# Optimization experiments

Hardware: AMD Instinct MI355X
Metric: run time of the kernel (lower is better)

## Reference

```python
import jax, jax.numpy as jnp
import numpy as np

N, E, G = 50000, 1600000, 8
IN, H, C = 64, 4, 32
HID = H * C  # 128
L = 3


def setup_inputs() -> dict:
    key = jax.random.key(0)
    ks = jax.random.split(key, 20)
    x = jax.random.normal(ks[0], (N, IN), dtype=jnp.float32)
    edge_index = jax.random.randint(ks[1], (2, E), 0, N, dtype=jnp.int64)
    batch = jnp.sort(jax.random.randint(ks[2], (N,), 0, G, dtype=jnp.int64))
    s = 0.05
    Wp = jax.random.normal(ks[3], (IN, HID), dtype=jnp.float32) * s
    bp = jnp.zeros((HID,), dtype=jnp.float32)
    Wl = jax.random.normal(ks[4], (L, HID, HID), dtype=jnp.float32) * s
    att_src = jax.random.normal(ks[5], (L, H, C), dtype=jnp.float32) * s
    att_dst = jax.random.normal(ks[6], (L, H, C), dtype=jnp.float32) * s
    bconv = jnp.zeros((L, HID), dtype=jnp.float32)
    W1 = jax.random.normal(ks[7], (2 * HID, 256), dtype=jnp.float32) * s
    b1 = jnp.zeros((256,), dtype=jnp.float32)
    W2 = jax.random.normal(ks[8], (256, 128), dtype=jnp.float32) * s
    b2 = jnp.zeros((128,), dtype=jnp.float32)
    W3 = jax.random.normal(ks[9], (128, 1), dtype=jnp.float32) * s
    b3 = jnp.zeros((1,), dtype=jnp.float32)
    return dict(x=x, edge_index=edge_index, batch=batch, Wp=Wp, bp=bp, Wl=Wl,
                att_src=att_src, att_dst=att_dst, bconv=bconv,
                W1=W1, b1=b1, W2=W2, b2=b2, W3=W3, b3=b3)


def _gat_layer(x, src, dst, W, a_src, a_dst, b):
    # PyG GATConv (concat=True, add_self_loops handled by caller via src/dst)
    h = (x @ W).reshape(N, H, C)                      # [N,H,C]
    asrc = jnp.sum(h * a_src, axis=-1)                # [N,H]
    adst = jnp.sum(h * a_dst, axis=-1)                # [N,H]
    e = jax.nn.leaky_relu(asrc[src] + adst[dst], 0.2)  # [E',H]
    m = jax.ops.segment_max(e, dst, num_segments=N)   # scatter-softmax over dst
    e = jnp.exp(e - m[dst])
    z = jax.ops.segment_sum(e, dst, num_segments=N)
    alpha = e / (z[dst] + 1e-16)                      # [E',H]
    out = jax.ops.segment_sum(h[src] * alpha[:, :, None], dst, num_segments=N)
    return out.reshape(N, HID) + b


def reference(x, edge_index, batch, Wp, bp, Wl, att_src, att_dst, bconv,
              W1, b1, W2, b2, W3, b3):
    # add self loops once (PyG default add_self_loops=True)
    loop = jnp.arange(N, dtype=edge_index.dtype)
    src = jnp.concatenate([edge_index[0], loop])
    dst = jnp.concatenate([edge_index[1], loop])

    h = jax.nn.relu(x @ Wp + bp)
    for l in range(L):
        h = jax.nn.relu(_gat_layer(h, src, dst, Wl[l], att_src[l], att_dst[l], bconv[l]))

    cnt = jax.ops.segment_sum(jnp.ones((N,), h.dtype), batch, num_segments=G)
    mean = jax.ops.segment_sum(h, batch, num_segments=G) / jnp.maximum(cnt, 1.0)[:, None]
    mx = jax.ops.segment_max(h, batch, num_segments=G)
    mx = jnp.where(cnt[:, None] > 0, mx, 0.0)
    p = jnp.concatenate([mean, mx], axis=-1)          # [G, 2*HID]

    p = jax.nn.relu(p @ W1 + b1)
    p = jax.nn.relu(p @ W2 + b2)
    return (p @ W3 + b3).squeeze(-1)                  # [G]
```

## Files before the change

kernel.cpp:

```cpp
#include <hip/hip_runtime.h>
#include <math.h>

#define NN 50000
#define GG 8
#define HEADS 4
#define CH 32
#define HID 128
#define NLAYER 3
#define POOL_S 64
#define DEG_CAP 96
#define NBG2 ((NN + 63) / 64)
#define NBS 1024

typedef __attribute__((ext_vector_type(8))) short bf16x8;
typedef __attribute__((ext_vector_type(4))) float f32x4;

__device__ float g_h[(size_t)NN * HID];
__device__ __attribute__((aligned(16))) unsigned short g_h2b[(size_t)NN * HID];
__device__ __attribute__((aligned(16))) unsigned short g_xhi[(size_t)NN * HID];
__device__ __attribute__((aligned(16))) unsigned short g_xlo[(size_t)NN * HID];
__device__ __attribute__((aligned(16))) unsigned short g_wthi[(size_t)NLAYER * HID * HID];
__device__ __attribute__((aligned(16))) unsigned short g_wtlo[(size_t)NLAYER * HID * HID];
__device__ float g_as[(size_t)NN * HEADS];
__device__ float g_ad[(size_t)NN * HEADS];
__device__ int g_cursor[NN];
__device__ __attribute__((aligned(16))) unsigned short g_csr16[(size_t)NN * DEG_CAP];
__device__ int g_starts[GG + 1];
__device__ double g_psum[(size_t)GG * POOL_S * HID];
__device__ float g_pmax[(size_t)GG * POOL_S * HID];

__device__ __forceinline__ float lrelu(float v) { return v > 0.f ? v : 0.2f * v; }

__device__ __forceinline__ float bf2f(unsigned short u) {
    union { unsigned int i; float f; } v;
    v.i = ((unsigned int)u) << 16;
    return v.f;
}
__device__ __forceinline__ unsigned short f2bf(float f) {
    union { float f; unsigned int i; } v;
    v.f = f;
    unsigned int r = v.i + 0x7FFFu + ((v.i >> 16) & 1u);
    return (unsigned short)(r >> 16);
}

__global__ void zero_kernel() {
    int i = blockIdx.x * blockDim.x + threadIdx.x;
    if (i < NN) g_cursor[i] = 0;
}

__global__ void wprep_kernel(const float* __restrict__ Wl) {
    int idx = blockIdx.x * 256 + threadIdx.x;
    if (idx >= NLAYER * HID * HID) return;
    int lay = idx / (HID * HID);
    int rem = idx - lay * HID * HID;
    int n = rem >> 7, k = rem & 127;
    float v = Wl[(size_t)lay * HID * HID + (size_t)k * HID + n];
    unsigned short h = f2bf(v);
    float r = v - bf2f(h);
    g_wthi[idx] = h;
    g_wtlo[idx] = f2bf(r);
}

template <int K>
__device__ __forceinline__ void proj_body(
    const float* __restrict__ Xp, const float* __restrict__ W, const float* __restrict__ bias,
    int blk) {
    constexpr int KT = 32;
    constexpr int XS = 68;
    __shared__ float Ws[KT * 128];
    __shared__ float Xs[KT * XS];
    int tid = threadIdx.x;
    int base = blk * 64;
    int rows = NN - base;
    if (rows > 64) rows = 64;
    int cg = tid & 15, rg = tid >> 4;
    int c0 = cg * 8, r0 = rg * 4;
    float acc[4][8];
#pragma unroll
    for (int i = 0; i < 4; i++)
#pragma unroll
        for (int j = 0; j < 8; j++) acc[i][j] = 0.f;

    for (int kb = 0; kb < K; kb += KT) {
        {
            const float4* Wg = (const float4*)(W + (size_t)kb * 128);
            float4* Ws4 = (float4*)Ws;
#pragma unroll
            for (int u = 0; u < 4; u++) Ws4[tid + u * 256] = Wg[tid + u * 256];
        }
#pragma unroll
        for (int u = 0; u < 2; u++) {
            int i = tid + u * 256;
            int r = i >> 3, k4 = i & 7;
            float4 v = {0.f, 0.f, 0.f, 0.f};
            if (r < rows) v = *(const float4*)(Xp + (size_t)(base + r) * K + kb + k4 * 4);
            Xs[(k4 * 4 + 0) * XS + r] = v.x;
            Xs[(k4 * 4 + 1) * XS + r] = v.y;
            Xs[(k4 * 4 + 2) * XS + r] = v.z;
            Xs[(k4 * 4 + 3) * XS + r] = v.w;
        }
        __syncthreads();
#pragma unroll 8
        for (int k = 0; k < KT; k++) {
            const float4 xa = *(const float4*)&Xs[k * XS + r0];
            const float4 wa = *(const float4*)&Ws[k * 128 + c0];
            const float4 wb = *(const float4*)&Ws[k * 128 + c0 + 4];
            const float xr[4] = {xa.x, xa.y, xa.z, xa.w};
            const float wr[8] = {wa.x, wa.y, wa.z, wa.w, wb.x, wb.y, wb.z, wb.w};
#pragma unroll
            for (int ii = 0; ii < 4; ii++)
#pragma unroll
                for (int jj = 0; jj < 8; jj++) acc[ii][jj] += xr[ii] * wr[jj];
        }
        __syncthreads();
    }

    float bv[8];
#pragma unroll
    for (int j = 0; j < 8; j++) bv[j] = bias[c0 + j];
#pragma unroll
    for (int ii = 0; ii < 4; ii++) {
        int r = r0 + ii;
        if (r < rows) {
            ushort4 h0, l0, h1, l1;
            float o[8];
#pragma unroll
            for (int jj = 0; jj < 8; jj++) o[jj] = fmaxf(acc[ii][jj] + bv[jj], 0.f);
            h0.x = f2bf(o[0]); h0.y = f2bf(o[1]); h0.z = f2bf(o[2]); h0.w = f2bf(o[3]);
            h1.x = f2bf(o[4]); h1.y = f2bf(o[5]); h1.z = f2bf(o[6]); h1.w = f2bf(o[7]);
            l0.x = f2bf(o[0] - bf2f(h0.x)); l0.y = f2bf(o[1] - bf2f(h0.y));
            l0.z = f2bf(o[2] - bf2f(h0.z)); l0.w = f2bf(o[3] - bf2f(h0.w));
            l1.x = f2bf(o[4] - bf2f(h1.x)); l1.y = f2bf(o[5] - bf2f(h1.y));
            l1.z = f2bf(o[6] - bf2f(h1.z)); l1.w = f2bf(o[7] - bf2f(h1.w));
            size_t off = (size_t)(base + r) * 128 + c0;
            *(ushort4*)&g_xhi[off] = h0;
            *(ushort4*)&g_xhi[off + 4] = h1;
            *(ushort4*)&g_xlo[off] = l0;
            *(ushort4*)&g_xlo[off + 4] = l1;
        }
    }
}

__device__ __forceinline__ void mfma_att_body(
    const float* __restrict__ att_s, const float* __restrict__ att_d,
    int lay, int blk) {
    __shared__ float Ysh[64][HID];
    int tid = threadIdx.x;
    int w = tid >> 6, l = tid & 63;
    int base = blk * 64;
    int rows = NN - base;
    if (rows > 64) rows = 64;
    int ar = l & 15, kg = l >> 4;
    int arow = base + w * 16 + ar;
    if (arow >= NN) arow = NN - 1;
    const unsigned short* xh = g_xhi + (size_t)arow * HID + kg * 8;
    const unsigned short* xl = g_xlo + (size_t)arow * HID + kg * 8;
    const unsigned short* wh = g_wthi + (size_t)lay * HID * HID + (size_t)ar * HID + kg * 8;
    const unsigned short* wl = g_wtlo + (size_t)lay * HID * HID + (size_t)ar * HID + kg * 8;

    f32x4 acc[8];
#pragma unroll
    for (int ct = 0; ct < 8; ct++) acc[ct] = (f32x4){0.f, 0.f, 0.f, 0.f};

#pragma unroll
    for (int ks = 0; ks < 4; ks++) {
        bf16x8 ah = *(const bf16x8*)(xh + ks * 32);
        bf16x8 al = *(const bf16x8*)(xl + ks * 32);
#pragma unroll
        for (int ct = 0; ct < 8; ct++) {
            bf16x8 bh = *(const bf16x8*)(wh + ct * 16 * HID + ks * 32);
            bf16x8 bl = *(const bf16x8*)(wl + ct * 16 * HID + ks * 32);
            acc[ct] = __builtin_amdgcn_mfma_f32_16x16x32_bf16(ah, bh, acc[ct], 0, 0, 0);
            acc[ct] = __builtin_amdgcn_mfma_f32_16x16x32_bf16(al, bh, acc[ct], 0, 0, 0);
            acc[ct] = __builtin_amdgcn_mfma_f32_16x16x32_bf16(ah, bl, acc[ct], 0, 0, 0);
        }
    }

#pragma unroll
    for (int ct = 0; ct < 8; ct++)
#pragma unroll
        for (int j = 0; j < 4; j++)
            Ysh[w * 16 + kg * 4 + j][ct * 16 + ar] = acc[ct][j];
    __syncthreads();

    int cg = tid & 15, rg = tid >> 4;
    int c0 = cg * 8, r0 = rg * 4;
    float avs[8], avd[8];
#pragma unroll
    for (int j = 0; j < 8; j++) { avs[j] = att_s[c0 + j]; avd[j] = att_d[c0 + j]; }
#pragma unroll
    for (int ii = 0; ii < 4; ii++) {
        int r = r0 + ii;
        float o[8];
#pragma unroll
        for (int jj = 0; jj < 8; jj++) o[jj] = Ysh[r][c0 + jj];
        if (r < rows) {
            uint4 pk;
            pk.x = (unsigned)f2bf(o[0]) | ((unsigned)f2bf(o[1]) << 16);
            pk.y = (unsigned)f2bf(o[2]) | ((unsigned)f2bf(o[3]) << 16);
            pk.z = (unsigned)f2bf(o[4]) | ((unsigned)f2bf(o[5]) << 16);
            pk.w = (unsigned)f2bf(o[6]) | ((unsigned)f2bf(o[7]) << 16);
            *(uint4*)&g_h2b[(size_t)(base + r) * 128 + c0] = pk;
        }
        float ps = 0.f, pd = 0.f;
#pragma unroll
        for (int jj = 0; jj < 8; jj++) { ps += o[jj] * avs[jj]; pd += o[jj] * avd[jj]; }
        ps += __shfl_xor(ps, 1); ps += __shfl_xor(ps, 2);
        pd += __shfl_xor(pd, 1); pd += __shfl_xor(pd, 2);
        if ((cg & 3) == 0 && r < rows) {
            g_as[(size_t)(base + r) * 4 + (cg >> 2)] = ps;
            g_ad[(size_t)(base + r) * 4 + (cg >> 2)] = pd;
        }
    }
}

__device__ __forceinline__ void scatter_body(
    const int* __restrict__ srcv, const int* __restrict__ dstv,
    int ebeg, int eend, int blk, int nblk) {
    int idx = ebeg + blk * 256 + threadIdx.x;
    int stride = nblk * 256;
    for (int j = idx; j < eend; j += stride) {
        int d = dstv[j];
        int pos = atomicAdd(&g_cursor[d], 1);
        if (pos < DEG_CAP) g_csr16[(size_t)d * DEG_CAP + pos] = (unsigned short)srcv[j];
    }
}

__global__ __launch_bounds__(256) void fat1_kernel(
    const float* __restrict__ Xp, const float* __restrict__ W, const float* __restrict__ bias,
    const int* __restrict__ srcv, const int* __restrict__ dstv, int ebeg, int eend) {
    if (blockIdx.x < NBG2) proj_body<64>(Xp, W, bias, blockIdx.x);
    else scatter_body(srcv, dstv, ebeg, eend, blockIdx.x - NBG2, gridDim.x - NBG2);
}

__global__ __launch_bounds__(256, 2) void fat2_kernel(
    const float* __restrict__ att_s, const float* __restrict__ att_d,
    const int* __restrict__ srcv, const int* __restrict__ dstv, int ebeg, int eend) {
    if (blockIdx.x < NBG2) mfma_att_body(att_s, att_d, 0, blockIdx.x);
    else scatter_body(srcv, dstv, ebeg, eend, blockIdx.x - NBG2, gridDim.x - NBG2);
}

__global__ __launch_bounds__(256, 2) void att_gemm_kernel(
    const float* __restrict__ att_s, const float* __restrict__ att_d, int lay) {
    mfma_att_body(att_s, att_d, lay, blockIdx.x);
}

template <bool LAST>
__global__ __launch_bounds__(256) void gat_layer_kernel(const float* __restrict__ bconv) {
    int wave = threadIdx.x >> 6;
    int lane = threadIdx.x & 63;
    int i = blockIdx.x * 4 + wave;

    int deg = g_cursor[i];
    if (deg > DEG_CAP) deg = DEG_CAP;

    int stream = lane >> 5;
    int sl = lane & 31;
    int hl = sl >> 3;
    int li = sl & 7;
    int c0 = sl * 4;
    int bsel = lane & 56;

    float ad_h = g_ad[(size_t)i * 4 + hl];
    const unsigned short* csr = &g_csr16[(size_t)i * DEG_CAP];

    float4 acc = {0.f, 0.f, 0.f, 0.f};
    float zraw = 0.f;

    int nfull = deg >> 4;
    for (int t = 0; t < nfull; ++t) {
        int j0 = t * 16 + stream * 8;
        uint4 cs = *(const uint4*)(csr + j0);
        int s0 = cs.x & 0xFFFF, s1 = cs.x >> 16;
        int s2 = cs.y & 0xFFFF, s3 = cs.y >> 16;
        int s4 = cs.z & 0xFFFF, s5 = cs.z >> 16;
        int s6 = cs.w & 0xFFFF, s7 = cs.w >> 16;
        ushort4 q0 = *(const ushort4*)&g_h2b[(s0 << 7) + c0];
        ushort4 q1 = *(const ushort4*)&g_h2b[(s1 << 7) + c0];
        ushort4 q2 = *(const ushort4*)&g_h2b[(s2 << 7) + c0];
        ushort4 q3 = *(const ushort4*)&g_h2b[(s3 << 7) + c0];
        ushort4 q4 = *(const ushort4*)&g_h2b[(s4 << 7) + c0];
        ushort4 q5 = *(const ushort4*)&g_h2b[(s5 << 7) + c0];
        ushort4 q6 = *(const ushort4*)&g_h2b[(s6 << 7) + c0];
        ushort4 q7 = *(const ushort4*)&g_h2b[(s7 << 7) + c0];
        unsigned wsel = li < 4 ? (li < 2 ? cs.x : cs.y) : (li < 6 ? cs.z : cs.w);
        int sm = (li & 1) ? (int)(wsel >> 16) : (int)(wsel & 0xFFFF);
        float a = g_as[(sm << 2) + hl];
        float wr = expf(lrelu(a + ad_h));
        zraw += wr;
        float w0 = __shfl(wr, bsel | 0);
        float w1 = __shfl(wr, bsel | 1);
        float w2 = __shfl(wr, bsel | 2);
        float w3 = __shfl(wr, bsel | 3);
        float w4 = __shfl(wr, bsel | 4);
        float w5 = __shfl(wr, bsel | 5);
        float w6 = __shfl(wr, bsel | 6);
        float w7 = __shfl(wr, bsel | 7);
        acc.x += w0 * bf2f(q0.x); acc.y += w0 * bf2f(q0.y); acc.z += w0 * bf2f(q0.z); acc.w += w0 * bf2f(q0.w);
        acc.x += w1 * bf2f(q1.x); acc.y += w1 * bf2f(q1.y); acc.z += w1 * bf2f(q1.z); acc.w += w1 * bf2f(q1.w);
        acc.x += w2 * bf2f(q2.x); acc.y += w2 * bf2f(q2.y); acc.z += w2 * bf2f(q2.z); acc.w += w2 * bf2f(q2.w);
        acc.x += w3 * bf2f(q3.x); acc.y += w3 * bf2f(q3.y); acc.z += w3 * bf2f(q3.z); acc.w += w3 * bf2f(q3.w);
        acc.x += w4 * bf2f(q4.x); acc.y += w4 * bf2f(q4.y); acc.z += w4 * bf2f(q4.z); acc.w += w4 * bf2f(q4.w);
        acc.x += w5 * bf2f(q5.x); acc.y += w5 * bf2f(q5.y); acc.z += w5 * bf2f(q5.z); acc.w += w5 * bf2f(q5.w);
        acc.x += w6 * bf2f(q6.x); acc.y += w6 * bf2f(q6.y); acc.z += w6 * bf2f(q6.z); acc.w += w6 * bf2f(q6.w);
        acc.x += w7 * bf2f(q7.x); acc.y += w7 * bf2f(q7.y); acc.z += w7 * bf2f(q7.z); acc.w += w7 * bf2f(q7.w);
    }

    int tbase = nfull * 16 + stream * 8;
#pragma unroll
    for (int k = 0; k < 8; ++k) {
        if (tbase + k < deg) {
            int s = csr[tbase + k];
            float a = g_as[(s << 2) + hl];
            float wr = expf(lrelu(a + ad_h));
            zraw += wr * 0.125f;
            ushort4 q = *(const ushort4*)&g_h2b[(s << 7) + c0];
            acc.x += wr * bf2f(q.x); acc.y += wr * bf2f(q.y);
            acc.z += wr * bf2f(q.z); acc.w += wr * bf2f(q.w);
        }
    }

    acc.x += __shfl_xor(acc.x, 32);
    acc.y += __shfl_xor(acc.y, 32);
    acc.z += __shfl_xor(acc.z, 32);
    acc.w += __shfl_xor(acc.w, 32);
    zraw += __shfl_xor(zraw, 1);
    zraw += __shfl_xor(zraw, 2);
    zraw += __shfl_xor(zraw, 4);
    zraw += __shfl_xor(zraw, 32);

    if (lane < 32) {
        float as_i = g_as[(i << 2) + hl];
        float sw = expf(lrelu(as_i + ad_h));
        float invz = 1.f / (zraw + sw + 1e-16f);
        ushort4 qs = *(const ushort4*)&g_h2b[(i << 7) + c0];
        float4 bc = *(const float4*)&bconv[c0];
        float4 o;
        o.x = fmaxf((sw * bf2f(qs.x) + acc.x) * invz + bc.x, 0.f);
        o.y = fmaxf((sw * bf2f(qs.y) + acc.y) * invz + bc.y, 0.f);
        o.z = fmaxf((sw * bf2f(qs.z) + acc.z) * invz + bc.z, 0.f);
        o.w = fmaxf((sw * bf2f(qs.w) + acc.w) * invz + bc.w, 0.f);
        if (LAST) {
            *(float4*)&g_h[(size_t)i * 128 + c0] = o;
        } else {
            ushort4 hh, ll;
            hh.x = f2bf(o.x); hh.y = f2bf(o.y); hh.z = f2bf(o.z); hh.w = f2bf(o.w);
            ll.x = f2bf(o.x - bf2f(hh.x)); ll.y = f2bf(o.y - bf2f(hh.y));
            ll.z = f2bf(o.z - bf2f(hh.z)); ll.w = f2bf(o.w - bf2f(hh.w));
            *(ushort4*)&g_xhi[(size_t)i * 128 + c0] = hh;
            *(ushort4*)&g_xlo[(size_t)i * 128 + c0] = ll;
        }
    }
}

__global__ void bounds_kernel(const int* __restrict__ batch) {
    int t = threadIdx.x;
    if (t > GG) return;
    int lo = 0, hi = NN;
    while (lo < hi) {
        int mid = (lo + hi) >> 1;
        if (batch[mid] < t) lo = mid + 1; else hi = mid;
    }
    g_starts[t] = lo;
}

__global__ void pool1_kernel() {
    int g = blockIdx.x / POOL_S, s = blockIdx.x % POOL_S;
    int n0 = g_starts[g], n1 = g_starts[g + 1];
    long long cnt = n1 - n0;
    int a = n0 + (int)(cnt * s / POOL_S);
    int b = n0 + (int)(cnt * (s + 1) / POOL_S);
    int c = threadIdx.x;
    double sum = 0.0;
    float mx = -INFINITY;
    for (int nn = a; nn < b; nn++) {
        float v = g_h[(size_t)nn * 128 + c];
        sum += v;
        mx = fmaxf(mx, v);
    }
    g_psum[(size_t)blockIdx.x * 128 + c] = sum;
    g_pmax[(size_t)blockIdx.x * 128 + c] = mx;
}

__global__ __launch_bounds__(256) void head_kernel(
    const float* __restrict__ W1, const float* __restrict__ b1,
    const float* __restrict__ W2, const float* __restrict__ b2,
    const float* __restrict__ W3, const float* __restrict__ b3,
    float* __restrict__ outv) {
    __shared__ float p[256];
    __shared__ float r1[256];
    __shared__ float r2[128];
    int g = blockIdx.x, t = threadIdx.x;
    int cnt = g_starts[g + 1] - g_starts[g];
    if (t < 128) {
        double s = 0.0;
        for (int q = 0; q < POOL_S; q++) s += g_psum[(size_t)(g * POOL_S + q) * 128 + t];
        double dcnt = cnt > 0 ? (double)cnt : 1.0;
        p[t] = (float)(s / dcnt);
    } else {
        int c = t - 128;
        float mx = -INFINITY;
        for (int q = 0; q < POOL_S; q++) mx = fmaxf(mx, g_pmax[(size_t)(g * POOL_S + q) * 128 + c]);
        p[t] = cnt > 0 ? mx : 0.f;
    }
    __syncthreads();
    float acc = b1[t];
    for (int k = 0; k < 256; k++) acc += p[k] * W1[k * 256 + t];
    r1[t] = fmaxf(acc, 0.f);
    __syncthreads();
    if (t < 128) {
        float a2 = b2[t];
        for (int k = 0; k < 256; k++) a2 += r1[k] * W2[k * 128 + t];
        r2[t] = fmaxf(a2, 0.f);
    }
    __syncthreads();
    if (t < 64) {
        float a3 = r2[t] * W3[t] + r2[t + 64] * W3[t + 64];
#pragma unroll
        for (int d = 32; d >= 1; d >>= 1) a3 += __shfl_down(a3, d);
        if (t == 0) outv[g] = a3 + b3[0];
    }
}

extern "C" void kernel_launch(void* const* d_in, const int* in_sizes, int n_in,
                              void* d_out, int out_size, void* d_ws, size_t ws_size,
                              hipStream_t stream) {
    const float* x = (const float*)d_in[0];
    const int* eidx = (const int*)d_in[1];
    const int* batch = (const int*)d_in[2];
    const float* Wp = (const float*)d_in[3];
    const float* bp = (const float*)d_in[4];
    const float* Wl = (const float*)d_in[5];
    const float* att_src = (const float*)d_in[6];
    const float* att_dst = (const float*)d_in[7];
    const float* bconv = (const float*)d_in[8];
    const float* W1 = (const float*)d_in[9];
    const float* b1 = (const float*)d_in[10];
    const float* W2 = (const float*)d_in[11];
    const float* b2 = (const float*)d_in[12];
    const float* W3 = (const float*)d_in[13];
    const float* b3 = (const float*)d_in[14];
    float* out = (float*)d_out;
    int E = in_sizes[1] / 2;
    int Emid = E / 2;

    zero_kernel<<<(NN + 255) / 256, 256, 0, stream>>>();
    wprep_kernel<<<(NLAYER * HID * HID + 255) / 256, 256, 0, stream>>>(Wl);

    fat1_kernel<<<NBG2 + NBS, 256, 0, stream>>>(x, Wp, bp, eidx, eidx + E, 0, Emid);

    fat2_kernel<<<NBG2 + NBS, 256, 0, stream>>>(att_src, att_dst, eidx, eidx + E, Emid, E);

    gat_layer_kernel<false><<<NN / 4, 256, 0, stream>>>(bconv);

    att_gemm_kernel<<<NBG2, 256, 0, stream>>>(
        att_src + (size_t)1 * HEADS * CH, att_dst + (size_t)1 * HEADS * CH, 1);
    gat_layer_kernel<false><<<NN / 4, 256, 0, stream>>>(bconv + (size_t)1 * HID);

    att_gemm_kernel<<<NBG2, 256, 0, stream>>>(
        att_src + (size_t)2 * HEADS * CH, att_dst + (size_t)2 * HEADS * CH, 2);
    gat_layer_kernel<true><<<NN / 4, 256, 0, stream>>>(bconv + (size_t)2 * HID);

    bounds_kernel<<<1, 64, 0, stream>>>(batch);
    pool1_kernel<<<GG * POOL_S, 128, 0, stream>>>();
    head_kernel<<<GG, 256, 0, stream>>>(W1, b1, W2, b2, W3, b3, out);
}
```

Measured before the change: 541.4 us.

## Split GAT aggregation per head with one wave per node-head pair

Changes the GAT aggregation work mapping so each wave handles one node and one head instead of one node and all heads. The grid grows fourfold. Each lane computes one edge's attention weight once, then shares the source ids and weights through shuffles while eight edge groups gather 32-channel slices. This removes the redundant per-head exp computations and aims for more parallelism and better latency hiding, at the cost of four times more CSR reads and more shuffle reductions. CSR index stores and loads also become nontemporal.

```diff
diff --git a/kernel.cpp b/kernel.cpp
--- a/kernel.cpp
+++ b/kernel.cpp
@@ -222,7 +222,8 @@
     for (int j = idx; j < eend; j += stride) {
         int d = dstv[j];
         int pos = atomicAdd(&g_cursor[d], 1);
-        if (pos < DEG_CAP) g_csr16[(size_t)d * DEG_CAP + pos] = (unsigned short)srcv[j];
+        if (pos < DEG_CAP)
+            __builtin_nontemporal_store((unsigned short)srcv[j], &g_csr16[(size_t)d * DEG_CAP + pos]);
     }
 }
 
@@ -249,106 +250,99 @@
 __global__ __launch_bounds__(256) void gat_layer_kernel(const float* __restrict__ bconv) {
     int wave = threadIdx.x >> 6;
     int lane = threadIdx.x & 63;
-    int i = blockIdx.x * 4 + wave;
+    int h = blockIdx.x & 3;
+    int i = (blockIdx.x >> 2) * 4 + wave;
 
     int deg = g_cursor[i];
     if (deg > DEG_CAP) deg = DEG_CAP;
 
-    int stream = lane >> 5;
-    int sl = lane & 31;
-    int hl = sl >> 3;
-    int li = sl & 7;
-    int c0 = sl * 4;
-    int bsel = lane & 56;
-
-    float ad_h = g_ad[(size_t)i * 4 + hl];
+    int li = lane & 7;
+    int e = lane >> 3;
+    int cb = (h << 5) + (li << 2);
+
+    float ad_h = g_ad[(size_t)i * 4 + h];
     const unsigned short* csr = &g_csr16[(size_t)i * DEG_CAP];
 
     float4 acc = {0.f, 0.f, 0.f, 0.f};
-    float zraw = 0.f;
-
-    int nfull = deg >> 4;
-    for (int t = 0; t < nfull; ++t) {
-        int j0 = t * 16 + stream * 8;
-        uint4 cs = *(const uint4*)(csr + j0);
-        int s0 = cs.x & 0xFFFF, s1 = cs.x >> 16;
-        int s2 = cs.y & 0xFFFF, s3 = cs.y >> 16;
-        int s4 = cs.z & 0xFFFF, s5 = cs.z >> 16;
-        int s6 = cs.w & 0xFFFF, s7 = cs.w >> 16;
-        ushort4 q0 = *(const ushort4*)&g_h2b[(s0 << 7) + c0];
-        ushort4 q1 = *(const ushort4*)&g_h2b[(s1 << 7) + c0];
-        ushort4 q2 = *(const ushort4*)&g_h2b[(s2 << 7) + c0];
-        ushort4 q3 = *(const ushort4*)&g_h2b[(s3 << 7) + c0];
-        ushort4 q4 = *(const ushort4*)&g_h2b[(s4 << 7) + c0];
-        ushort4 q5 = *(const ushort4*)&g_h2b[(s5 << 7) + c0];
-        ushort4 q6 = *(const ushort4*)&g_h2b[(s6 << 7) + c0];
-        ushort4 q7 = *(const ushort4*)&g_h2b[(s7 << 7) + c0];
-        unsigned wsel = li < 4 ? (li < 2 ? cs.x : cs.y) : (li < 6 ? cs.z : cs.w);
-        int sm = (li & 1) ? (int)(wsel >> 16) : (int)(wsel & 0xFFFF);
-        float a = g_as[(sm << 2) + hl];
-        float wr = expf(lrelu(a + ad_h));
-        zraw += wr;
-        float w0 = __shfl(wr, bsel | 0);
-        float w1 = __shfl(wr, bsel | 1);
-        float w2 = __shfl(wr, bsel | 2);
-        float w3 = __shfl(wr, bsel | 3);
-        float w4 = __shfl(wr, bsel | 4);
-        float w5 = __shfl(wr, bsel | 5);
-        float w6 = __shfl(wr, bsel | 6);
-        float w7 = __shfl(wr, bsel | 7);
-        acc.x += w0 * bf2f(q0.x); acc.y += w0 * bf2f(q0.y); acc.z += w0 * bf2f(q0.z); acc.w += w0 * bf2f(q0.w);
-        acc.x += w1 * bf2f(q1.x); acc.y += w1 * bf2f(q1.y); acc.z += w1 * bf2f(q1.z); acc.w += w1 * bf2f(q1.w);
-        acc.x += w2 * bf2f(q2.x); acc.y += w2 * bf2f(q2.y); acc.z += w2 * bf2f(q2.z); acc.w += w2 * bf2f(q2.w);
-        acc.x += w3 * bf2f(q3.x); acc.y += w3 * bf2f(q3.y); acc.z += w3 * bf2f(q3.z); acc.w += w3 * bf2f(q3.w);
-        acc.x += w4 * bf2f(q4.x); acc.y += w4 * bf2f(q4.y); acc.z += w4 * bf2f(q4.z); acc.w += w4 * bf2f(q4.w);
-        acc.x += w5 * bf2f(q5.x); acc.y += w5 * bf2f(q5.y); acc.z += w5 * bf2f(q5.z); acc.w += w5 * bf2f(q5.w);
-        acc.x += w6 * bf2f(q6.x); acc.y += w6 * bf2f(q6.y); acc.z += w6 * bf2f(q6.z); acc.w += w6 * bf2f(q6.w);
-        acc.x += w7 * bf2f(q7.x); acc.y += w7 * bf2f(q7.y); acc.z += w7 * bf2f(q7.z); acc.w += w7 * bf2f(q7.w);
-    }
-
-    int tbase = nfull * 16 + stream * 8;
-#pragma unroll
-    for (int k = 0; k < 8; ++k) {
-        if (tbase + k < deg) {
-            int s = csr[tbase + k];
-            float a = g_as[(s << 2) + hl];
-            float wr = expf(lrelu(a + ad_h));
-            zraw += wr * 0.125f;
-            ushort4 q = *(const ushort4*)&g_h2b[(s << 7) + c0];
-            acc.x += wr * bf2f(q.x); acc.y += wr * bf2f(q.y);
-            acc.z += wr * bf2f(q.z); acc.w += wr * bf2f(q.w);
-        }
-    }
-
-    acc.x += __shfl_xor(acc.x, 32);
-    acc.y += __shfl_xor(acc.y, 32);
-    acc.z += __shfl_xor(acc.z, 32);
-    acc.w += __shfl_xor(acc.w, 32);
-    zraw += __shfl_xor(zraw, 1);
-    zraw += __shfl_xor(zraw, 2);
-    zraw += __shfl_xor(zraw, 4);
-    zraw += __shfl_xor(zraw, 32);
-
-    if (lane < 32) {
-        float as_i = g_as[(i << 2) + hl];
+    float z = 0.f;
+
+#pragma unroll
+    for (int p = 0; p < 2; ++p) {
+        int base = p << 6;
+        int cnt = deg - base;
+        if (cnt <= 0) break;
+        if (cnt > 64) cnt = 64;
+        int myid = 0;
+        float wv = 0.f;
+        if (lane < cnt) {
+            myid = __builtin_nontemporal_load(&csr[base + lane]);
+            float a = g_as[(myid << 2) + h];
+            wv = expf(lrelu(a + ad_h));
+        }
+        z += wv;
+        int nr = (cnt + 7) >> 3;
+        int r = 0;
+        for (; r + 4 <= (cnt >> 3); r += 4) {
+            int j0 = r * 8 + e;
+            int s0 = __shfl(myid, j0);
+            int s1 = __shfl(myid, j0 + 8);
+            int s2 = __shfl(myid, j0 + 16);
+            int s3 = __shfl(myid, j0 + 24);
+            float w0 = __shfl(wv, j0);
+            float w1 = __shfl(wv, j0 + 8);
+            float w2 = __shfl(wv, j0 + 16);
+            float w3 = __shfl(wv, j0 + 24);
+            ushort4 q0 = *(const ushort4*)&g_h2b[(s0 << 7) + cb];
+            ushort4 q1 = *(const ushort4*)&g_h2b[(s1 << 7) + cb];
+            ushort4 q2 = *(const ushort4*)&g_h2b[(s2 << 7) + cb];
+            ushort4 q3 = *(const ushort4*)&g_h2b[(s3 << 7) + cb];
+            acc.x += w0 * bf2f(q0.x); acc.y += w0 * bf2f(q0.y); acc.z += w0 * bf2f(q0.z); acc.w += w0 * bf2f(q0.w);
+            acc.x += w1 * bf2f(q1.x); acc.y += w1 * bf2f(q1.y); acc.z += w1 * bf2f(q1.z); acc.w += w1 * bf2f(q1.w);
+            acc.x += w2 * bf2f(q2.x); acc.y += w2 * bf2f(q2.y); acc.z += w2 * bf2f(q2.z); acc.w += w2 * bf2f(q2.w);
+            acc.x += w3 * bf2f(q3.x); acc.y += w3 * bf2f(q3.y); acc.z += w3 * bf2f(q3.z); acc.w += w3 * bf2f(q3.w);
+        }
+        for (; r < nr; ++r) {
+            int j = r * 8 + e;
+            int s = __shfl(myid, j);
+            float w = __shfl(wv, j);
+            if (j < cnt) {
+                ushort4 q = *(const ushort4*)&g_h2b[(s << 7) + cb];
+                acc.x += w * bf2f(q.x); acc.y += w * bf2f(q.y);
+                acc.z += w * bf2f(q.z); acc.w += w * bf2f(q.w);
+            }
+        }
+    }
+
+    acc.x += __shfl_xor(acc.x, 8);  acc.y += __shfl_xor(acc.y, 8);
+    acc.z += __shfl_xor(acc.z, 8);  acc.w += __shfl_xor(acc.w, 8);
+    acc.x += __shfl_xor(acc.x, 16); acc.y += __shfl_xor(acc.y, 16);
+    acc.z += __shfl_xor(acc.z, 16); acc.w += __shfl_xor(acc.w, 16);
+    acc.x += __shfl_xor(acc.x, 32); acc.y += __shfl_xor(acc.y, 32);
+    acc.z += __shfl_xor(acc.z, 32); acc.w += __shfl_xor(acc.w, 32);
+    z += __shfl_xor(z, 1);  z += __shfl_xor(z, 2);  z += __shfl_xor(z, 4);
+    z += __shfl_xor(z, 8);  z += __shfl_xor(z, 16); z += __shfl_xor(z, 32);
+
+    if (lane < 8) {
+        float as_i = g_as[(i << 2) + h];
         float sw = expf(lrelu(as_i + ad_h));
-        float invz = 1.f / (zraw + sw + 1e-16f);
-        ushort4 qs = *(const ushort4*)&g_h2b[(i << 7) + c0];
-        float4 bc = *(const float4*)&bconv[c0];
+        float invz = 1.f / (z + sw + 1e-16f);
+        int co = (h << 5) + (lane << 2);
+        ushort4 qs = *(const ushort4*)&g_h2b[(i << 7) + co];
+        float4 bc = *(const float4*)&bconv[co];
         float4 o;
         o.x = fmaxf((sw * bf2f(qs.x) + acc.x) * invz + bc.x, 0.f);
         o.y = fmaxf((sw * bf2f(qs.y) + acc.y) * invz + bc.y, 0.f);
         o.z = fmaxf((sw * bf2f(qs.z) + acc.z) * invz + bc.z, 0.f);
         o.w = fmaxf((sw * bf2f(qs.w) + acc.w) * invz + bc.w, 0.f);
         if (LAST) {
-            *(float4*)&g_h[(size_t)i * 128 + c0] = o;
+            *(float4*)&g_h[(size_t)i * 128 + co] = o;
         } else {
             ushort4 hh, ll;
             hh.x = f2bf(o.x); hh.y = f2bf(o.y); hh.z = f2bf(o.z); hh.w = f2bf(o.w);
             ll.x = f2bf(o.x - bf2f(hh.x)); ll.y = f2bf(o.y - bf2f(hh.y));
             ll.z = f2bf(o.z - bf2f(hh.z)); ll.w = f2bf(o.w - bf2f(hh.w));
-            *(ushort4*)&g_xhi[(size_t)i * 128 + c0] = hh;
-            *(ushort4*)&g_xlo[(size_t)i * 128 + c0] = ll;
+            *(ushort4*)&g_xhi[(size_t)i * 128 + co] = hh;
+            *(ushort4*)&g_xlo[(size_t)i * 128 + co] = ll;
         }
     }
 }
@@ -451,15 +445,15 @@
 
     fat2_kernel<<<NBG2 + NBS, 256, 0, stream>>>(att_src, att_dst, eidx, eidx + E, Emid, E);
 
-    gat_layer_kernel<false><<<NN / 4, 256, 0, stream>>>(bconv);
+    gat_layer_kernel<false><<<NN, 256, 0, stream>>>(bconv);
 
     att_gemm_kernel<<<NBG2, 256, 0, stream>>>(
         att_src + (size_t)1 * HEADS * CH, att_dst + (size_t)1 * HEADS * CH, 1);
-    gat_layer_kernel<false><<<NN / 4, 256, 0, stream>>>(bconv + (size_t)1 * HID);
+    gat_layer_kernel<false><<<NN, 256, 0, stream>>>(bconv + (size_t)1 * HID);
 
     att_gemm_kernel<<<NBG2, 256, 0, stream>>>(
         att_src + (size_t)2 * HEADS * CH, att_dst + (size_t)2 * HEADS * CH, 2);
-    gat_layer_kernel<true><<<NN / 4, 256, 0, stream>>>(bconv + (size_t)2 * HID);
+    gat_layer_kernel<true><<<NN, 256, 0, stream>>>(bconv + (size_t)2 * HID);
 
     bounds_kernel<<<1, 64, 0, stream>>>(batch);
     pool1_kernel<<<GG * POOL_S, 128, 0, stream>>>();
```

Result: slower. 819.2 us (+51.3%).

## Fuse next-layer projection and attention scores into GAT aggregation kernel

Applied to the files above, without the earlier changes.

The separate MFMA projection kernel for layers 2 and 3 is removed. Each aggregation block now keeps its 4 output rows in shared memory and multiplies them by the next layer's weight matrix with scalar FP32 FMAs. It writes the bf16 features and attention logits into ping-pong buffers. This avoids writing and re-reading the split hi/lo activations and saves two launches. In exchange, every block reloads the full 128x128 weight matrix from global memory for only 4 rows, and the matmul runs on CUDA-core FMAs instead of MFMA.

```diff
diff --git a/kernel.cpp b/kernel.cpp
--- a/kernel.cpp
+++ b/kernel.cpp
@@ -16,13 +16,16 @@
 typedef __attribute__((ext_vector_type(4))) float f32x4;
 
 __device__ float g_h[(size_t)NN * HID];
-__device__ __attribute__((aligned(16))) unsigned short g_h2b[(size_t)NN * HID];
+__device__ __attribute__((aligned(16))) unsigned short g_h2bA[(size_t)NN * HID];
+__device__ __attribute__((aligned(16))) unsigned short g_h2bB[(size_t)NN * HID];
 __device__ __attribute__((aligned(16))) unsigned short g_xhi[(size_t)NN * HID];
 __device__ __attribute__((aligned(16))) unsigned short g_xlo[(size_t)NN * HID];
-__device__ __attribute__((aligned(16))) unsigned short g_wthi[(size_t)NLAYER * HID * HID];
-__device__ __attribute__((aligned(16))) unsigned short g_wtlo[(size_t)NLAYER * HID * HID];
-__device__ float g_as[(size_t)NN * HEADS];
-__device__ float g_ad[(size_t)NN * HEADS];
+__device__ __attribute__((aligned(16))) unsigned short g_wthi[(size_t)HID * HID];
+__device__ __attribute__((aligned(16))) unsigned short g_wtlo[(size_t)HID * HID];
+__device__ float g_asA[(size_t)NN * HEADS];
+__device__ float g_asB[(size_t)NN * HEADS];
+__device__ float g_adA[(size_t)NN * HEADS];
+__device__ float g_adB[(size_t)NN * HEADS];
 __device__ int g_cursor[NN];
 __device__ __attribute__((aligned(16))) unsigned short g_csr16[(size_t)NN * DEG_CAP];
 __device__ int g_starts[GG + 1];
@@ -50,11 +53,9 @@
 
 __global__ void wprep_kernel(const float* __restrict__ Wl) {
     int idx = blockIdx.x * 256 + threadIdx.x;
-    if (idx >= NLAYER * HID * HID) return;
-    int lay = idx / (HID * HID);
-    int rem = idx - lay * HID * HID;
-    int n = rem >> 7, k = rem & 127;
-    float v = Wl[(size_t)lay * HID * HID + (size_t)k * HID + n];
+    if (idx >= HID * HID) return;
+    int n = idx >> 7, k = idx & 127;
+    float v = Wl[(size_t)k * HID + n];
     unsigned short h = f2bf(v);
     float r = v - bf2f(h);
     g_wthi[idx] = h;
@@ -142,8 +143,7 @@
 }
 
 __device__ __forceinline__ void mfma_att_body(
-    const float* __restrict__ att_s, const float* __restrict__ att_d,
-    int lay, int blk) {
+    const float* __restrict__ att_s, const float* __restrict__ att_d, int blk) {
     __shared__ float Ysh[64][HID];
     int tid = threadIdx.x;
     int w = tid >> 6, l = tid & 63;
@@ -155,8 +155,8 @@
     if (arow >= NN) arow = NN - 1;
     const unsigned short* xh = g_xhi + (size_t)arow * HID + kg * 8;
     const unsigned short* xl = g_xlo + (size_t)arow * HID + kg * 8;
-    const unsigned short* wh = g_wthi + (size_t)lay * HID * HID + (size_t)ar * HID + kg * 8;
-    const unsigned short* wl = g_wtlo + (size_t)lay * HID * HID + (size_t)ar * HID + kg * 8;
+    const unsigned short* wh = g_wthi + (size_t)ar * HID + kg * 8;
+    const unsigned short* wl = g_wtlo + (size_t)ar * HID + kg * 8;
 
     f32x4 acc[8];
 #pragma unroll
@@ -200,7 +200,7 @@
             pk.y = (unsigned)f2bf(o[2]) | ((unsigned)f2bf(o[3]) << 16);
             pk.z = (unsigned)f2bf(o[4]) | ((unsigned)f2bf(o[5]) << 16);
             pk.w = (unsigned)f2bf(o[6]) | ((unsigned)f2bf(o[7]) << 16);
-            *(uint4*)&g_h2b[(size_t)(base + r) * 128 + c0] = pk;
+            *(uint4*)&g_h2bA[(size_t)(base + r) * 128 + c0] = pk;
         }
         float ps = 0.f, pd = 0.f;
 #pragma unroll
@@ -208,8 +208,8 @@
         ps += __shfl_xor(ps, 1); ps += __shfl_xor(ps, 2);
         pd += __shfl_xor(pd, 1); pd += __shfl_xor(pd, 2);
         if ((cg & 3) == 0 && r < rows) {
-            g_as[(size_t)(base + r) * 4 + (cg >> 2)] = ps;
-            g_ad[(size_t)(base + r) * 4 + (cg >> 2)] = pd;
+            g_asA[(size_t)(base + r) * 4 + (cg >> 2)] = ps;
+            g_adA[(size_t)(base + r) * 4 + (cg >> 2)] = pd;
         }
     }
 }
@@ -236,17 +236,25 @@
 __global__ __launch_bounds__(256, 2) void fat2_kernel(
     const float* __restrict__ att_s, const float* __restrict__ att_d,
     const int* __restrict__ srcv, const int* __restrict__ dstv, int ebeg, int eend) {
-    if (blockIdx.x < NBG2) mfma_att_body(att_s, att_d, 0, blockIdx.x);
+    if (blockIdx.x < NBG2) mfma_att_body(att_s, att_d, blockIdx.x);
     else scatter_body(srcv, dstv, ebeg, eend, blockIdx.x - NBG2, gridDim.x - NBG2);
 }
 
-__global__ __launch_bounds__(256, 2) void att_gemm_kernel(
-    const float* __restrict__ att_s, const float* __restrict__ att_d, int lay) {
-    mfma_att_body(att_s, att_d, lay, blockIdx.x);
-}
-
-template <bool LAST>
-__global__ __launch_bounds__(256) void gat_layer_kernel(const float* __restrict__ bconv) {
+template <int INBUF, bool LAST>
+__global__ __launch_bounds__(256) void gat_layer_kernel(
+    const float* __restrict__ bconv,
+    const float* __restrict__ attS_next, const float* __restrict__ attD_next,
+    const float* __restrict__ Wnext) {
+    const unsigned short* h2b = (INBUF == 0) ? g_h2bA : g_h2bB;
+    unsigned short* h2b_out = (INBUF == 0) ? g_h2bB : g_h2bA;
+    const float* as_in = (INBUF == 0) ? g_asA : g_asB;
+    const float* ad_in = (INBUF == 0) ? g_adA : g_adB;
+    float* as_out = (INBUF == 0) ? g_asB : g_asA;
+    float* ad_out = (INBUF == 0) ? g_adB : g_adA;
+
+    __shared__ float osh[4][HID];
+    __shared__ float Wsh[16][HID];
+
     int wave = threadIdx.x >> 6;
     int lane = threadIdx.x & 63;
     int i = blockIdx.x * 4 + wave;
@@ -261,7 +269,7 @@
     int c0 = sl * 4;
     int bsel = lane & 56;
 
-    float ad_h = g_ad[(size_t)i * 4 + hl];
+    float ad_h = ad_in[(size_t)i * 4 + hl];
     const unsigned short* csr = &g_csr16[(size_t)i * DEG_CAP];
 
     float4 acc = {0.f, 0.f, 0.f, 0.f};
@@ -275,17 +283,17 @@
         int s2 = cs.y & 0xFFFF, s3 = cs.y >> 16;
         int s4 = cs.z & 0xFFFF, s5 = cs.z >> 16;
         int s6 = cs.w & 0xFFFF, s7 = cs.w >> 16;
-        ushort4 q0 = *(const ushort4*)&g_h2b[(s0 << 7) + c0];
-        ushort4 q1 = *(const ushort4*)&g_h2b[(s1 << 7) + c0];
-        ushort4 q2 = *(const ushort4*)&g_h2b[(s2 << 7) + c0];
-        ushort4 q3 = *(const ushort4*)&g_h2b[(s3 << 7) + c0];
-        ushort4 q4 = *(const ushort4*)&g_h2b[(s4 << 7) + c0];
-        ushort4 q5 = *(const ushort4*)&g_h2b[(s5 << 7) + c0];
-        ushort4 q6 = *(const ushort4*)&g_h2b[(s6 << 7) + c0];
-        ushort4 q7 = *(const ushort4*)&g_h2b[(s7 << 7) + c0];
+        ushort4 q0 = *(const ushort4*)&h2b[(s0 << 7) + c0];
+        ushort4 q1 = *(const ushort4*)&h2b[(s1 << 7) + c0];
+        ushort4 q2 = *(const ushort4*)&h2b[(s2 << 7) + c0];
+        ushort4 q3 = *(const ushort4*)&h2b[(s3 << 7) + c0];
+        ushort4 q4 = *(const ushort4*)&h2b[(s4 << 7) + c0];
+        ushort4 q5 = *(const ushort4*)&h2b[(s5 << 7) + c0];
+        ushort4 q6 = *(const ushort4*)&h2b[(s6 << 7) + c0];
+        ushort4 q7 = *(const ushort4*)&h2b[(s7 << 7) + c0];
         unsigned wsel = li < 4 ? (li < 2 ? cs.x : cs.y) : (li < 6 ? cs.z : cs.w);
         int sm = (li & 1) ? (int)(wsel >> 16) : (int)(wsel & 0xFFFF);
-        float a = g_as[(sm << 2) + hl];
+        float a = as_in[(sm << 2) + hl];
         float wr = expf(lrelu(a + ad_h));
         zraw += wr;
         float w0 = __shfl(wr, bsel | 0);
@@ -311,10 +319,10 @@
     for (int k = 0; k < 8; ++k) {
         if (tbase + k < deg) {
             int s = csr[tbase + k];
-            float a = g_as[(s << 2) + hl];
+            float a = as_in[(s << 2) + hl];
             float wr = expf(lrelu(a + ad_h));
             zraw += wr * 0.125f;
-            ushort4 q = *(const ushort4*)&g_h2b[(s << 7) + c0];
+            ushort4 q = *(const ushort4*)&h2b[(s << 7) + c0];
             acc.x += wr * bf2f(q.x); acc.y += wr * bf2f(q.y);
             acc.z += wr * bf2f(q.z); acc.w += wr * bf2f(q.w);
         }
@@ -330,10 +338,10 @@
     zraw += __shfl_xor(zraw, 32);
 
     if (lane < 32) {
-        float as_i = g_as[(i << 2) + hl];
+        float as_i = as_in[(i << 2) + hl];
         float sw = expf(lrelu(as_i + ad_h));
         float invz = 1.f / (zraw + sw + 1e-16f);
-        ushort4 qs = *(const ushort4*)&g_h2b[(i << 7) + c0];
+        ushort4 qs = *(const ushort4*)&h2b[(i << 7) + c0];
         float4 bc = *(const float4*)&bconv[c0];
         float4 o;
         o.x = fmaxf((sw * bf2f(qs.x) + acc.x) * invz + bc.x, 0.f);
@@ -343,12 +351,48 @@
         if (LAST) {
             *(float4*)&g_h[(size_t)i * 128 + c0] = o;
         } else {
-            ushort4 hh, ll;
-            hh.x = f2bf(o.x); hh.y = f2bf(o.y); hh.z = f2bf(o.z); hh.w = f2bf(o.w);
-            ll.x = f2bf(o.x - bf2f(hh.x)); ll.y = f2bf(o.y - bf2f(hh.y));
-            ll.z = f2bf(o.z - bf2f(hh.z)); ll.w = f2bf(o.w - bf2f(hh.w));
-            *(ushort4*)&g_xhi[(size_t)i * 128 + c0] = hh;
-            *(ushort4*)&g_xlo[(size_t)i * 128 + c0] = ll;
+            *(float4*)&osh[wave][c0] = o;
+        }
+    }
+
+    if constexpr (!LAST) {
+        __syncthreads();
+        int t = threadIdx.x;
+        int c = t & 127, gg = t >> 7;
+        float y0 = 0.f, y1 = 0.f;
+        for (int kc = 0; kc < 8; ++kc) {
+#pragma unroll
+            for (int u = 0; u < 2; ++u) {
+                int idx = t + u * 256;
+                int kk = idx >> 5, nn = (idx & 31) << 2;
+                *(float4*)&Wsh[kk][nn] = *(const float4*)&Wnext[(size_t)(kc * 16 + kk) * HID + nn];
+            }
+            __syncthreads();
+#pragma unroll
+            for (int k = 0; k < 16; ++k) {
+                float wv = Wsh[k][c];
+                y0 += osh[gg * 2 + 0][kc * 16 + k] * wv;
+                y1 += osh[gg * 2 + 1][kc * 16 + k] * wv;
+            }
+            __syncthreads();
+        }
+        int node0 = blockIdx.x * 4;
+        h2b_out[(size_t)(node0 + gg * 2 + 0) * HID + c] = f2bf(y0);
+        h2b_out[(size_t)(node0 + gg * 2 + 1) * HID + c] = f2bf(y1);
+        float sa = attS_next[c], da = attD_next[c];
+        float ps0 = y0 * sa, pd0 = y0 * da;
+        float ps1 = y1 * sa, pd1 = y1 * da;
+#pragma unroll
+        for (int m = 1; m < 32; m <<= 1) {
+            ps0 += __shfl_xor(ps0, m); pd0 += __shfl_xor(pd0, m);
+            ps1 += __shfl_xor(ps1, m); pd1 += __shfl_xor(pd1, m);
+        }
+        if ((t & 31) == 0) {
+            int hh = c >> 5;
+            as_out[(size_t)(node0 + gg * 2 + 0) * 4 + hh] = ps0;
+            ad_out[(size_t)(node0 + gg * 2 + 0) * 4 + hh] = pd0;
+            as_out[(size_t)(node0 + gg * 2 + 1) * 4 + hh] = ps1;
+            ad_out[(size_t)(node0 + gg * 2 + 1) * 4 + hh] = pd1;
         }
     }
 }
@@ -445,21 +489,21 @@
     int Emid = E / 2;
 
     zero_kernel<<<(NN + 255) / 256, 256, 0, stream>>>();
-    wprep_kernel<<<(NLAYER * HID * HID + 255) / 256, 256, 0, stream>>>(Wl);
+    wprep_kernel<<<(HID * HID + 255) / 256, 256, 0, stream>>>(Wl);
 
     fat1_kernel<<<NBG2 + NBS, 256, 0, stream>>>(x, Wp, bp, eidx, eidx + E, 0, Emid);
 
     fat2_kernel<<<NBG2 + NBS, 256, 0, stream>>>(att_src, att_dst, eidx, eidx + E, Emid, E);
 
-    gat_layer_kernel<false><<<NN / 4, 256, 0, stream>>>(bconv);
-
-    att_gemm_kernel<<<NBG2, 256, 0, stream>>>(
-        att_src + (size_t)1 * HEADS * CH, att_dst + (size_t)1 * HEADS * CH, 1);
-    gat_layer_kernel<false><<<NN / 4, 256, 0, stream>>>(bconv + (size_t)1 * HID);
-
-    att_gemm_kernel<<<NBG2, 256, 0, stream>>>(
-        att_src + (size_t)2 * HEADS * CH, att_dst + (size_t)2 * HEADS * CH, 2);
-    gat_layer_kernel<true><<<NN / 4, 256, 0, stream>>>(bconv + (size_t)2 * HID);
+    gat_layer_kernel<0, false><<<NN / 4, 256, 0, stream>>>(
+        bconv, att_src + (size_t)1 * HID, att_dst + (size_t)1 * HID, Wl + (size_t)1 * HID * HID);
+
+    gat_layer_kernel<1, false><<<NN / 4, 256, 0, stream>>>(
+        bconv + (size_t)1 * HID, att_src + (size_t)2 * HID, att_dst + (size_t)2 * HID,
+        Wl + (size_t)2 * HID * HID);
+
+    gat_layer_kernel<0, true><<<NN / 4, 256, 0, stream>>>(
+        bconv + (size_t)2 * HID, nullptr, nullptr, nullptr);
 
     bounds_kernel<<<1, 64, 0, stream>>>(batch);
     pool1_kernel<<<GG * POOL_S, 128, 0, stream>>>();
```

Measured after the change: 596.7 us. 10.2% more time.

## Build CSR via two-pass bucket binning with shared-memory slices

Applied to the files above, without the earlier changes.

Replaces the per-edge global atomic scatter into the padded CSR with a two-pass build. Edges are first binned into 128-node buckets, each split into four sub-segments, using one global atomic per edge on a small cursor array. A second kernel then assembles each bucket's CSR slice in LDS and writes it out with coalesced 16-byte stores. This targets the random atomics and scattered 2-byte writes across a large array, at the cost of an extra kernel, an intermediate buffer, and a fixed per-bucket capacity (SEGCAP) that silently drops edges if exceeded. The layer-0 attention GEMM is no longer fused with the scatter and now runs as a separate launch.

```diff
diff --git a/kernel.cpp b/kernel.cpp
--- a/kernel.cpp
+++ b/kernel.cpp
@@ -11,6 +11,8 @@
 #define DEG_CAP 96
 #define NBG2 ((NN + 63) / 64)
 #define NBS 1024
+#define NBKT ((NN + 127) / 128)
+#define SEGCAP 1536
 
 typedef __attribute__((ext_vector_type(8))) short bf16x8;
 typedef __attribute__((ext_vector_type(4))) float f32x4;
@@ -25,6 +27,8 @@
 __device__ float g_ad[(size_t)NN * HEADS];
 __device__ int g_cursor[NN];
 __device__ __attribute__((aligned(16))) unsigned short g_csr16[(size_t)NN * DEG_CAP];
+__device__ int g_bcur[NBKT * 4];
+__device__ unsigned g_bbuf[(size_t)NBKT * 4 * SEGCAP];
 __device__ int g_starts[GG + 1];
 __device__ double g_psum[(size_t)GG * POOL_S * HID];
 __device__ float g_pmax[(size_t)GG * POOL_S * HID];
@@ -45,7 +49,7 @@
 
 __global__ void zero_kernel() {
     int i = blockIdx.x * blockDim.x + threadIdx.x;
-    if (i < NN) g_cursor[i] = 0;
+    if (i < NBKT * 4) g_bcur[i] = 0;
 }
 
 __global__ void wprep_kernel(const float* __restrict__ Wl) {
@@ -141,12 +145,63 @@
     }
 }
 
-__device__ __forceinline__ void mfma_att_body(
-    const float* __restrict__ att_s, const float* __restrict__ att_d,
-    int lay, int blk) {
+__device__ __forceinline__ void bin_body(
+    const int* __restrict__ srcv, const int* __restrict__ dstv, int E, int blk, int nblk) {
+    int idx = blk * 256 + threadIdx.x;
+    int stride = nblk * 256;
+    int seg3 = blk & 3;
+    for (int j = idx; j < E; j += stride) {
+        int d = dstv[j];
+        int s = srcv[j];
+        int seg = ((d >> 7) << 2) | seg3;
+        int pos = atomicAdd(&g_bcur[seg], 1);
+        if (pos < SEGCAP)
+            g_bbuf[(size_t)seg * SEGCAP + pos] = (unsigned)s | ((unsigned)(d & 127) << 16);
+    }
+}
+
+__global__ __launch_bounds__(256) void fat1_kernel(
+    const float* __restrict__ Xp, const float* __restrict__ W, const float* __restrict__ bias,
+    const int* __restrict__ srcv, const int* __restrict__ dstv, int E) {
+    if (blockIdx.x < NBG2) proj_body<64>(Xp, W, bias, blockIdx.x);
+    else bin_body(srcv, dstv, E, blockIdx.x - NBG2, NBS);
+}
+
+__global__ __launch_bounds__(256) void csr_build_kernel() {
+    __shared__ __attribute__((aligned(16))) unsigned short slice[128 * DEG_CAP];
+    __shared__ int lcur[128];
+    int b = blockIdx.x, tid = threadIdx.x;
+    if (tid < 128) lcur[tid] = 0;
+    __syncthreads();
+#pragma unroll
+    for (int sgi = 0; sgi < 4; ++sgi) {
+        int seg = (b << 2) | sgi;
+        int n = g_bcur[seg];
+        if (n > SEGCAP) n = SEGCAP;
+        for (int j = tid; j < n; j += 256) {
+            unsigned e = g_bbuf[(size_t)seg * SEGCAP + j];
+            int nl = e >> 16;
+            int p = atomicAdd(&lcur[nl], 1);
+            if (p < DEG_CAP) slice[nl * DEG_CAP + p] = (unsigned short)(e & 0xFFFF);
+        }
+    }
+    __syncthreads();
+    int base = b * 128;
+    int nodes = NN - base;
+    if (nodes > 128) nodes = 128;
+    if (tid < nodes) g_cursor[base + tid] = lcur[tid];
+    int tot = nodes * (DEG_CAP / 8);
+    uint4* dst4 = (uint4*)&g_csr16[(size_t)base * DEG_CAP];
+    const uint4* src4 = (const uint4*)slice;
+    for (int t = tid; t < tot; t += 256) dst4[t] = src4[t];
+}
+
+__global__ __launch_bounds__(256, 2) void att_gemm_kernel(
+    const float* __restrict__ att_s, const float* __restrict__ att_d, int lay) {
     __shared__ float Ysh[64][HID];
     int tid = threadIdx.x;
     int w = tid >> 6, l = tid & 63;
+    int blk = blockIdx.x;
     int base = blk * 64;
     int rows = NN - base;
     if (rows > 64) rows = 64;
@@ -212,37 +267,6 @@
             g_ad[(size_t)(base + r) * 4 + (cg >> 2)] = pd;
         }
     }
-}
-
-__device__ __forceinline__ void scatter_body(
-    const int* __restrict__ srcv, const int* __restrict__ dstv,
-    int ebeg, int eend, int blk, int nblk) {
-    int idx = ebeg + blk * 256 + threadIdx.x;
-    int stride = nblk * 256;
-    for (int j = idx; j < eend; j += stride) {
-        int d = dstv[j];
-        int pos = atomicAdd(&g_cursor[d], 1);
-        if (pos < DEG_CAP) g_csr16[(size_t)d * DEG_CAP + pos] = (unsigned short)srcv[j];
-    }
-}
-
-__global__ __launch_bounds__(256) void fat1_kernel(
-    const float* __restrict__ Xp, const float* __restrict__ W, const float* __restrict__ bias,
-    const int* __restrict__ srcv, const int* __restrict__ dstv, int ebeg, int eend) {
-    if (blockIdx.x < NBG2) proj_body<64>(Xp, W, bias, blockIdx.x);
-    else scatter_body(srcv, dstv, ebeg, eend, blockIdx.x - NBG2, gridDim.x - NBG2);
-}
-
-__global__ __launch_bounds__(256, 2) void fat2_kernel(
-    const float* __restrict__ att_s, const float* __restrict__ att_d,
-    const int* __restrict__ srcv, const int* __restrict__ dstv, int ebeg, int eend) {
-    if (blockIdx.x < NBG2) mfma_att_body(att_s, att_d, 0, blockIdx.x);
-    else scatter_body(srcv, dstv, ebeg, eend, blockIdx.x - NBG2, gridDim.x - NBG2);
-}
-
-__global__ __launch_bounds__(256, 2) void att_gemm_kernel(
-    const float* __restrict__ att_s, const float* __restrict__ att_d, int lay) {
-    mfma_att_body(att_s, att_d, lay, blockIdx.x);
 }
 
 template <bool LAST>
@@ -442,23 +466,23 @@
     const float* b3 = (const float*)d_in[14];
     float* out = (float*)d_out;
     int E = in_sizes[1] / 2;
-    int Emid = E / 2;
-
-    zero_kernel<<<(NN + 255) / 256, 256, 0, stream>>>();
+
+    zero_kernel<<<(NBKT * 4 + 255) / 256, 256, 0, stream>>>();
     wprep_kernel<<<(NLAYER * HID * HID + 255) / 256, 256, 0, stream>>>(Wl);
 
-    fat1_kernel<<<NBG2 + NBS, 256, 0, stream>>>(x, Wp, bp, eidx, eidx + E, 0, Emid);
-
-    fat2_kernel<<<NBG2 + NBS, 256, 0, stream>>>(att_src, att_dst, eidx, eidx + E, Emid, E);
-
+    fat1_kernel<<<NBG2 + NBS, 256, 0, stream>>>(x, Wp, bp, eidx, eidx + E, E);
+
+    csr_build_kernel<<<NBKT, 256, 0, stream>>>();
+
+    att_gemm_kernel<<<NBG2, 256, 0, stream>>>(att_src, att_dst, 0);
     gat_layer_kernel<false><<<NN / 4, 256, 0, stream>>>(bconv);
 
     att_gemm_kernel<<<NBG2, 256, 0, stream>>>(
-        att_src + (size_t)1 * HEADS * CH, att_dst + (size_t)1 * HEADS * CH, 1);
+        att_src + (size_t)1 * HID, att_dst + (size_t)1 * HID, 1);
     gat_layer_kernel<false><<<NN / 4, 256, 0, stream>>>(bconv + (size_t)1 * HID);
 
     att_gemm_kernel<<<NBG2, 256, 0, stream>>>(
-        att_src + (size_t)2 * HEADS * CH, att_dst + (size_t)2 * HEADS * CH, 2);
+        att_src + (size_t)2 * HID, att_dst + (size_t)2 * HID, 2);
     gat_layer_kernel<true><<<NN / 4, 256, 0, stream>>>(bconv + (size_t)2 * HID);
 
     bounds_kernel<<<1, 64, 0, stream>>>(batch);
```

Measured after the change: 742.3 us. +37.1%, slower.
